# Kernel tuning notes

Measured on AMD Instinct MI355X. Metric: run time of the kernel, lower is better.

The kernel has to match this reference:

```python
import jax, jax.numpy as jnp
import numpy as np

HEADS = 16
D_K = 64  # hidden_units // heads


def setup_inputs() -> dict:
    key = jax.random.key(0)
    ks = jax.random.split(key, 9)
    B, S, D, H = 4, 2048, 1024, 1024  # batch, seq, in_shape, hidden_units
    inputs = jax.random.normal(ks[0], (B, S, D), dtype=jnp.float32)
    # xavier_normal for weights, default bias init ~ small uniform (use zeros for simplicity of baseline? keep uniform like torch)
    def xavier(k, fan_in, fan_out):
        std = jnp.sqrt(2.0 / (fan_in + fan_out))
        return jax.random.normal(k, (fan_out, fan_in), dtype=jnp.float32) * std
    Wq = xavier(ks[1], D, H)
    Wk = xavier(ks[2], D, H)
    Wv = xavier(ks[3], D, H)
    Wo = xavier(ks[4], H, H)
    bound = 1.0 / jnp.sqrt(D)
    bq = jax.random.uniform(ks[5], (H,), minval=-bound, maxval=bound, dtype=jnp.float32)
    bk = jax.random.uniform(ks[6], (H,), minval=-bound, maxval=bound, dtype=jnp.float32)
    bv = jax.random.uniform(ks[7], (H,), minval=-bound, maxval=bound, dtype=jnp.float32)
    bo = jax.random.uniform(ks[8], (H,), minval=-1.0 / jnp.sqrt(H), maxval=1.0 / jnp.sqrt(H), dtype=jnp.float32)
    return {"inputs": inputs, "Wq": Wq, "bq": bq, "Wk": Wk, "bk": bk,
            "Wv": Wv, "bv": bv, "Wo": Wo, "bo": bo}


def reference(inputs, Wq, bq, Wk, bk, Wv, bv, Wo, bo):
    B, S, _ = inputs.shape
    # QKV projections -> (B, S, heads, d_k)
    def proj(W, b):
        return (inputs @ W.T + b).reshape(B, S, HEADS, D_K)
    q = proj(Wq, bq)
    k = proj(Wk, bk)
    v = proj(Wv, bv)
    scale = 1.0 / jnp.sqrt(jnp.float32(D_K))
    # scores: (B, heads, S, S)
    scores = jnp.einsum('bqhd,bkhd->bhqk', q, k) * scale
    attn = jax.nn.softmax(scores, axis=-1)
    # (B, heads, S, d_k) -> (B, S, heads*d_k)
    ctx = jnp.einsum('bhqk,bkhd->bqhd', attn, v).reshape(B, S, HEADS * D_K)
    out = ctx @ Wo.T + bo
    return out
```

## Files before the change

### kernel.cpp

```cpp
#include <hip/hip_runtime.h>
#include <stdint.h>


using bf16x8 = __attribute__((ext_vector_type(8))) short;
using f32x4  = __attribute__((ext_vector_type(4))) float;

#define QSCALE 0.18033688f

__device__ __forceinline__ unsigned short f2bf(float f) {
    unsigned u = __builtin_bit_cast(unsigned, f);
    u += 0x7fffu + ((u >> 16) & 1u);
    return (unsigned short)(u >> 16);
}

__device__ __forceinline__ unsigned pack2bf(float f0, float f1) {
    unsigned u0 = __builtin_bit_cast(unsigned, f0) + 0x8000u;
    unsigned u1 = __builtin_bit_cast(unsigned, f1) + 0x8000u;
    return __builtin_amdgcn_perm(u1, u0, 0x07060302);
}

__device__ __forceinline__ void gld16(const void* g, void* l) {
    void* gnc = (void*)g;
    __builtin_amdgcn_global_load_lds((__attribute__((address_space(1))) void*)gnc,
                                     (__attribute__((address_space(3))) void*)l,
                                     16, 0, 0);
}

__device__ __forceinline__ int swz(int R, int g) {
    return R * 64 + ((g ^ (R & 7)) << 3);
}

__global__ void castall(const float* __restrict__ X, const float* __restrict__ Wq,
                        const float* __restrict__ Wk, const float* __restrict__ Wv,
                        const float* __restrict__ Wo, unsigned short* __restrict__ Xb,
                        unsigned short* __restrict__ Wqkvb, unsigned short* __restrict__ Wob) {
    const int bx = blockIdx.x;
    const float* src; unsigned short* dst; int idx;
    if (bx < 8192) { src = X; dst = Xb; idx = bx * 256 + threadIdx.x; }
    else {
        const int r = bx - 8192, w = r >> 10;
        idx = (r & 1023) * 256 + threadIdx.x;
        src = (w == 0) ? Wq : (w == 1) ? Wk : (w == 2) ? Wv : Wo;
        dst = (w == 3) ? Wob : Wqkvb + (size_t)w * 1048576;
    }
    float4 v = ((const float4*)src)[idx];
    ((uint2*)dst)[idx] = make_uint2(pack2bf(v.x, v.y), pack2bf(v.z, v.w));
}

__global__ __launch_bounds__(256) void gemm_qkv(const unsigned short* __restrict__ A,
                                                const unsigned short* __restrict__ Wqkv,
                                                const float* __restrict__ bq,
                                                const float* __restrict__ bk,
                                                const float* __restrict__ bv,
                                                unsigned short* __restrict__ Qb,
                                                unsigned short* __restrict__ Kb,
                                                unsigned short* __restrict__ Vt) {
    __shared__ alignas(16) unsigned short smem[17408];
    unsigned short* sA = smem;
    unsigned short* sB = smem + 8192;
    unsigned short* OT = smem;

    const int tid  = threadIdx.x;
    const int lane = tid & 63;
    const int wave = tid >> 6;
    const int quad = lane >> 4;
    const int l15  = lane & 15;
    const int lr   = lane >> 3;
    const int lcs  = (((lane & 7) ^ lr) << 3);
    const int nb   = blockIdx.x >> 3;
    const int col0 = (blockIdx.x & 7) * 128;
    const int row0 = blockIdx.y * 128;
    const unsigned short* W = Wqkv + ((size_t)nb << 20);
    const float* bias = (nb == 0) ? bq : (nb == 1) ? bk : bv;
    const int wm = wave >> 1, wn = wave & 1;

    f32x4 acc[4][4];
#pragma unroll
    for (int i = 0; i < 4; i++)
#pragma unroll
        for (int j = 0; j < 4; j++) acc[i][j] = f32x4{0.f, 0.f, 0.f, 0.f};

    for (int kt = 0; kt < 16; ++kt) {
        const int k0 = kt * 64;
#pragma unroll
        for (int i = 0; i < 4; i++) {
            const int c = wave * 4 + i;
            const int r = c * 8 + lr;
            gld16(A + (size_t)(row0 + r) * 1024 + k0 + lcs, &sA[c * 512]);
            gld16(W + (size_t)(col0 + r) * 1024 + k0 + lcs, &sB[c * 512]);
        }
        __syncthreads();
#pragma unroll
        for (int kx = 0; kx < 2; ++kx) {
            bf16x8 a[4], b[4];
#pragma unroll
            for (int i = 0; i < 4; i++) {
                a[i] = *(const bf16x8*)&sA[swz(wm * 64 + i * 16 + l15, kx * 4 + quad)];
                b[i] = *(const bf16x8*)&sB[swz(wn * 64 + i * 16 + l15, kx * 4 + quad)];
            }
#pragma unroll
            for (int i = 0; i < 4; i++)
#pragma unroll
                for (int j = 0; j < 4; j++)
                    acc[i][j] = __builtin_amdgcn_mfma_f32_16x16x32_bf16(a[i], b[j], acc[i][j], 0, 0, 0);
        }
        __syncthreads();
    }

    if (nb != 2) {
        const float sc = (nb == 0) ? QSCALE : 1.0f;
#pragma unroll
        for (int i = 0; i < 4; i++) {
#pragma unroll
            for (int j = 0; j < 4; j++) {
                const int ct  = wn * 64 + j * 16 + l15;
                const float bvv = bias[col0 + ct];
                const int rt  = wm * 64 + i * 16 + quad * 4;
#pragma unroll
                for (int r = 0; r < 4; r++)
                    OT[(rt + r) * 136 + ct] = f2bf((acc[i][j][r] + bvv) * sc);
            }
        }
    } else {
#pragma unroll
        for (int i = 0; i < 4; i++) {
#pragma unroll
            for (int j = 0; j < 4; j++) {
                const int ct  = wn * 64 + j * 16 + l15;
                const float bvv = bias[col0 + ct];
                const int rt  = wm * 64 + i * 16 + quad * 4;
                *(uint2*)&OT[ct * 136 + rt] =
                    make_uint2(pack2bf(acc[i][j][0] + bvv, acc[i][j][1] + bvv),
                               pack2bf(acc[i][j][2] + bvv, acc[i][j][3] + bvv));
            }
        }
    }
    __syncthreads();

    const int rr   = wave * 32 + (lane >> 1);
    const int half = lane & 1;
    if (nb != 2) {
        unsigned short* C = (nb == 0) ? Qb : Kb;
        unsigned short* gdst = C + (size_t)(row0 + rr) * 1024 + col0 + half * 64;
#pragma unroll
        for (int k = 0; k < 8; k++)
            *(bf16x8*)(gdst + k * 8) = *(const bf16x8*)&OT[rr * 136 + half * 64 + k * 8];
    } else {
        const int bb = row0 >> 11, s0l = row0 & 2047;
        unsigned short* gdst = Vt + ((size_t)(bb * 1024 + col0 + rr)) * 2048 + s0l + half * 64;
#pragma unroll
        for (int k = 0; k < 8; k++)
            *(bf16x8*)(gdst + k * 8) = *(const bf16x8*)&OT[rr * 136 + half * 64 + k * 8];
    }
}

__global__ __launch_bounds__(256) void gemm_out(const unsigned short* __restrict__ A,
                                                const unsigned short* __restrict__ W,
                                                const float* __restrict__ bias,
                                                float* __restrict__ C) {
    __shared__ alignas(16) unsigned short sA[128 * 64];
    __shared__ alignas(16) unsigned short sB[128 * 64];
    const int tid  = threadIdx.x;
    const int lane = tid & 63;
    const int wave = tid >> 6;
    const int quad = lane >> 4;
    const int l15  = lane & 15;
    const int lr   = lane >> 3;
    const int lcs  = (((lane & 7) ^ lr) << 3);
    const int row0 = blockIdx.y * 128;
    const int col0 = blockIdx.x * 128;
    const int wm = wave >> 1, wn = wave & 1;

    f32x4 acc[4][4];
#pragma unroll
    for (int i = 0; i < 4; i++)
#pragma unroll
        for (int j = 0; j < 4; j++) acc[i][j] = f32x4{0.f, 0.f, 0.f, 0.f};

    for (int kt = 0; kt < 16; ++kt) {
        const int k0 = kt * 64;
#pragma unroll
        for (int i = 0; i < 4; i++) {
            const int c = wave * 4 + i;
            const int r = c * 8 + lr;
            gld16(A + (size_t)(row0 + r) * 1024 + k0 + lcs, &sA[c * 512]);
            gld16(W + (size_t)(col0 + r) * 1024 + k0 + lcs, &sB[c * 512]);
        }
        __syncthreads();
#pragma unroll
        for (int kx = 0; kx < 2; ++kx) {
            bf16x8 a[4], b[4];
#pragma unroll
            for (int i = 0; i < 4; i++) {
                a[i] = *(const bf16x8*)&sA[swz(wm * 64 + i * 16 + l15, kx * 4 + quad)];
                b[i] = *(const bf16x8*)&sB[swz(wn * 64 + i * 16 + l15, kx * 4 + quad)];
            }
#pragma unroll
            for (int i = 0; i < 4; i++)
#pragma unroll
                for (int j = 0; j < 4; j++)
                    acc[i][j] = __builtin_amdgcn_mfma_f32_16x16x32_bf16(a[i], b[j], acc[i][j], 0, 0, 0);
        }
        __syncthreads();
    }

#pragma unroll
    for (int i = 0; i < 4; i++) {
#pragma unroll
        for (int j = 0; j < 4; j++) {
            const int col   = col0 + wn * 64 + j * 16 + l15;
            const float bvv = bias[col];
            const int rbase = row0 + wm * 64 + i * 16 + quad * 4;
#pragma unroll
            for (int r = 0; r < 4; r++)
                C[(size_t)(rbase + r) * 1024 + col] = acc[i][j][r] + bvv;
        }
    }
}

__global__ __launch_bounds__(256) void attn(const unsigned short* __restrict__ Q,
                                            const unsigned short* __restrict__ K,
                                            const unsigned short* __restrict__ Vt,
                                            unsigned short* __restrict__ Ctx) {
    __shared__ alignas(16) unsigned short Kl[64 * 64];
    __shared__ alignas(16) unsigned short Vl[64 * 64];
    __shared__ alignas(16) unsigned short Pl[4][32][72];

    const int tid  = threadIdx.x;
    const int lane = tid & 63;
    const int wave = tid >> 6;
    const int quad = lane >> 4;
    const int l15  = lane & 15;
    const int lr   = lane >> 3;
    const int lcs  = (((lane & 7) ^ lr) << 3);

    const int qt = blockIdx.x, h = blockIdx.y, b = blockIdx.z;
    const int q0 = qt * 128;
    const size_t tokbase = (size_t)b * 2048;

    bf16x8 qa[2][2];
#pragma unroll
    for (int mt = 0; mt < 2; ++mt)
#pragma unroll
        for (int kx = 0; kx < 2; ++kx)
            qa[mt][kx] = *(const bf16x8*)(Q + (tokbase + q0 + wave * 32 + mt * 16 + l15) * 1024 +
                                          h * 64 + kx * 32 + quad * 8);

    f32x4 O[2][4];
#pragma unroll
    for (int mt = 0; mt < 2; ++mt)
#pragma unroll
        for (int nt = 0; nt < 4; ++nt) O[mt][nt] = f32x4{0.f, 0.f, 0.f, 0.f};
    float rs[2] = {0.f, 0.f};

    for (int kt = 0; kt < 32; ++kt) {
#pragma unroll
        for (int i = 0; i < 2; i++) {
            const int c  = wave * 2 + i;
            const int rr = c * 8 + lr;
            gld16(K + (tokbase + kt * 64 + rr) * 1024 + h * 64 + lcs, &Kl[c * 512]);
            gld16(Vt + ((size_t)(b * 1024 + h * 64 + rr)) * 2048 + kt * 64 + lcs, &Vl[c * 512]);
        }
        __syncthreads();

        f32x4 St[4][2];
#pragma unroll
        for (int nt = 0; nt < 4; ++nt)
#pragma unroll
            for (int mt = 0; mt < 2; ++mt) St[nt][mt] = f32x4{0.f, 0.f, 0.f, 0.f};
#pragma unroll
        for (int kx = 0; kx < 2; ++kx) {
            bf16x8 kb[4];
#pragma unroll
            for (int nt = 0; nt < 4; ++nt)
                kb[nt] = *(const bf16x8*)&Kl[swz(nt * 16 + l15, kx * 4 + quad)];
#pragma unroll
            for (int nt = 0; nt < 4; ++nt)
#pragma unroll
                for (int mt = 0; mt < 2; ++mt)
                    St[nt][mt] = __builtin_amdgcn_mfma_f32_16x16x32_bf16(kb[nt], qa[mt][kx], St[nt][mt], 0, 0, 0);
        }

#pragma unroll
        for (int mt = 0; mt < 2; ++mt) {
            float rsl = 0.f;
#pragma unroll
            for (int nt = 0; nt < 4; ++nt) {
                float p0 = __builtin_amdgcn_exp2f(St[nt][mt][0]);
                float p1 = __builtin_amdgcn_exp2f(St[nt][mt][1]);
                float p2 = __builtin_amdgcn_exp2f(St[nt][mt][2]);
                float p3 = __builtin_amdgcn_exp2f(St[nt][mt][3]);
                rsl += (p0 + p1) + (p2 + p3);
                *(uint2*)&Pl[wave][mt * 16 + l15][nt * 16 + quad * 4] =
                    make_uint2(pack2bf(p0, p1), pack2bf(p2, p3));
            }
            rs[mt] += rsl;
        }

#pragma unroll
        for (int kx = 0; kx < 2; ++kx) {
            bf16x8 pa[2], vb[4];
#pragma unroll
            for (int mt = 0; mt < 2; ++mt)
                pa[mt] = *(const bf16x8*)&Pl[wave][mt * 16 + l15][kx * 32 + quad * 8];
#pragma unroll
            for (int nt = 0; nt < 4; ++nt)
                vb[nt] = *(const bf16x8*)&Vl[swz(nt * 16 + l15, kx * 4 + quad)];
#pragma unroll
            for (int mt = 0; mt < 2; ++mt)
#pragma unroll
                for (int nt = 0; nt < 4; ++nt)
                    O[mt][nt] = __builtin_amdgcn_mfma_f32_16x16x32_bf16(pa[mt], vb[nt], O[mt][nt], 0, 0, 0);
        }
        __syncthreads();
    }

    float linv[2][4];
#pragma unroll
    for (int mt = 0; mt < 2; ++mt) {
        float lv = rs[mt];
        lv += __shfl_xor(lv, 16);
        lv += __shfl_xor(lv, 32);
#pragma unroll
        for (int r = 0; r < 4; ++r)
            linv[mt][r] = 1.0f / __shfl(lv, quad * 4 + r);
    }

#pragma unroll
    for (int mt = 0; mt < 2; ++mt) {
#pragma unroll
        for (int r = 0; r < 4; ++r) {
            const int row   = q0 + wave * 32 + mt * 16 + quad * 4 + r;
            const size_t base = (tokbase + row) * 1024 + h * 64;
#pragma unroll
            for (int nt = 0; nt < 4; ++nt)
                Ctx[base + nt * 16 + l15] = f2bf(O[mt][nt][r] * linv[mt][r]);
        }
    }
}

extern "C" void kernel_launch(void* const* d_in, const int* in_sizes, int n_in,
                              void* d_out, int out_size, void* d_ws, size_t ws_size,
                              hipStream_t stream) {
    (void)in_sizes; (void)n_in; (void)out_size; (void)ws_size;
    const float* X  = (const float*)d_in[0];
    const float* Wq = (const float*)d_in[1];
    const float* bq = (const float*)d_in[2];
    const float* Wk = (const float*)d_in[3];
    const float* bk = (const float*)d_in[4];
    const float* Wv = (const float*)d_in[5];
    const float* bv = (const float*)d_in[6];
    const float* Wo = (const float*)d_in[7];
    const float* bo = (const float*)d_in[8];

    char* ws = (char*)d_ws;
    unsigned short* Xb    = (unsigned short*)(ws);
    unsigned short* Qb    = (unsigned short*)(ws + (size_t)16 * 1048576);
    unsigned short* Kb    = (unsigned short*)(ws + (size_t)32 * 1048576);
    unsigned short* Vt    = (unsigned short*)(ws + (size_t)48 * 1048576);
    unsigned short* Wqkvb = (unsigned short*)(ws + (size_t)64 * 1048576);
    unsigned short* Wob   = (unsigned short*)(ws + (size_t)70 * 1048576);
    unsigned short* Ctx   = Xb;

    castall<<<dim3(12288), 256, 0, stream>>>(X, Wq, Wk, Wv, Wo, Xb, Wqkvb, Wob);
    gemm_qkv<<<dim3(24, 64), 256, 0, stream>>>(Xb, Wqkvb, bq, bk, bv, Qb, Kb, Vt);
    attn<<<dim3(16, 16, 4), 256, 0, stream>>>(Qb, Kb, Vt, Ctx);
    gemm_out<<<dim3(8, 64), 256, 0, stream>>>(Ctx, Wob, bo, (float*)d_out);
}
```

Before: 302.8 us.

## Double-buffer LDS tiles in output GEMM and attention kernels

Both gemm_out and attn now keep two LDS buffers and issue the global-to-LDS loads for the next K tile right after the barrier, before computing on the current tile. The trailing barrier is dropped, so each iteration has one barrier instead of two. The aim is to overlap global memory latency with MFMA work. It doubles LDS use per block, which may reduce occupancy. Correctness depends on the single barrier ordering buffer reuse and on the async LDS loads being complete when the barrier is reached.

```diff
diff --git a/kernel.cpp b/kernel.cpp
--- a/kernel.cpp
+++ b/kernel.cpp
@@ -158,8 +158,8 @@
                                                 const unsigned short* __restrict__ W,
                                                 const float* __restrict__ bias,
                                                 float* __restrict__ C) {
-    __shared__ alignas(16) unsigned short sA[128 * 64];
-    __shared__ alignas(16) unsigned short sB[128 * 64];
+    __shared__ alignas(16) unsigned short sA[2][8192];
+    __shared__ alignas(16) unsigned short sB[2][8192];
     const int tid  = threadIdx.x;
     const int lane = tid & 63;
     const int wave = tid >> 6;
@@ -177,23 +177,30 @@
 #pragma unroll
         for (int j = 0; j < 4; j++) acc[i][j] = f32x4{0.f, 0.f, 0.f, 0.f};
 
+#define GO_STAGE(kt_, buf_)                                                        \
+    {                                                                              \
+        const int k0_ = (kt_) * 64;                                                \
+        _Pragma("unroll")                                                          \
+        for (int i = 0; i < 4; i++) {                                              \
+            const int c = wave * 4 + i;                                            \
+            const int r = c * 8 + lr;                                              \
+            gld16(A + (size_t)(row0 + r) * 1024 + k0_ + lcs, &sA[buf_][c * 512]);  \
+            gld16(W + (size_t)(col0 + r) * 1024 + k0_ + lcs, &sB[buf_][c * 512]);  \
+        }                                                                          \
+    }
+
+    GO_STAGE(0, 0)
     for (int kt = 0; kt < 16; ++kt) {
-        const int k0 = kt * 64;
-#pragma unroll
-        for (int i = 0; i < 4; i++) {
-            const int c = wave * 4 + i;
-            const int r = c * 8 + lr;
-            gld16(A + (size_t)(row0 + r) * 1024 + k0 + lcs, &sA[c * 512]);
-            gld16(W + (size_t)(col0 + r) * 1024 + k0 + lcs, &sB[c * 512]);
-        }
+        const int buf = kt & 1;
         __syncthreads();
+        if (kt < 15) GO_STAGE(kt + 1, buf ^ 1)
 #pragma unroll
         for (int kx = 0; kx < 2; ++kx) {
             bf16x8 a[4], b[4];
 #pragma unroll
             for (int i = 0; i < 4; i++) {
-                a[i] = *(const bf16x8*)&sA[swz(wm * 64 + i * 16 + l15, kx * 4 + quad)];
-                b[i] = *(const bf16x8*)&sB[swz(wn * 64 + i * 16 + l15, kx * 4 + quad)];
+                a[i] = *(const bf16x8*)&sA[buf][swz(wm * 64 + i * 16 + l15, kx * 4 + quad)];
+                b[i] = *(const bf16x8*)&sB[buf][swz(wn * 64 + i * 16 + l15, kx * 4 + quad)];
             }
 #pragma unroll
             for (int i = 0; i < 4; i++)
@@ -201,8 +208,8 @@
                 for (int j = 0; j < 4; j++)
                     acc[i][j] = __builtin_amdgcn_mfma_f32_16x16x32_bf16(a[i], b[j], acc[i][j], 0, 0, 0);
         }
-        __syncthreads();
-    }
+    }
+#undef GO_STAGE
 
 #pragma unroll
     for (int i = 0; i < 4; i++) {
@@ -222,8 +229,8 @@
                                             const unsigned short* __restrict__ K,
                                             const unsigned short* __restrict__ Vt,
                                             unsigned short* __restrict__ Ctx) {
-    __shared__ alignas(16) unsigned short Kl[64 * 64];
-    __shared__ alignas(16) unsigned short Vl[64 * 64];
+    __shared__ alignas(16) unsigned short Kl[2][64 * 64];
+    __shared__ alignas(16) unsigned short Vl[2][64 * 64];
     __shared__ alignas(16) unsigned short Pl[4][32][72];
 
     const int tid  = threadIdx.x;
@@ -253,15 +260,23 @@
         for (int nt = 0; nt < 4; ++nt) O[mt][nt] = f32x4{0.f, 0.f, 0.f, 0.f};
     float rs[2] = {0.f, 0.f};
 
+#define AT_STAGE(kt_, buf_)                                                                     \
+    {                                                                                           \
+        _Pragma("unroll")                                                                       \
+        for (int i = 0; i < 2; i++) {                                                           \
+            const int c  = wave * 2 + i;                                                        \
+            const int rr = c * 8 + lr;                                                          \
+            gld16(K + (tokbase + (kt_) * 64 + rr) * 1024 + h * 64 + lcs, &Kl[buf_][c * 512]);   \
+            gld16(Vt + ((size_t)(b * 1024 + h * 64 + rr)) * 2048 + (kt_) * 64 + lcs,            \
+                  &Vl[buf_][c * 512]);                                                          \
+        }                                                                                       \
+    }
+
+    AT_STAGE(0, 0)
     for (int kt = 0; kt < 32; ++kt) {
-#pragma unroll
-        for (int i = 0; i < 2; i++) {
-            const int c  = wave * 2 + i;
-            const int rr = c * 8 + lr;
-            gld16(K + (tokbase + kt * 64 + rr) * 1024 + h * 64 + lcs, &Kl[c * 512]);
-            gld16(Vt + ((size_t)(b * 1024 + h * 64 + rr)) * 2048 + kt * 64 + lcs, &Vl[c * 512]);
-        }
+        const int buf = kt & 1;
         __syncthreads();
+        if (kt < 31) AT_STAGE(kt + 1, buf ^ 1)
 
         f32x4 St[4][2];
 #pragma unroll
@@ -273,7 +288,7 @@
             bf16x8 kb[4];
 #pragma unroll
             for (int nt = 0; nt < 4; ++nt)
-                kb[nt] = *(const bf16x8*)&Kl[swz(nt * 16 + l15, kx * 4 + quad)];
+                kb[nt] = *(const bf16x8*)&Kl[buf][swz(nt * 16 + l15, kx * 4 + quad)];
 #pragma unroll
             for (int nt = 0; nt < 4; ++nt)
 #pragma unroll
@@ -305,15 +320,15 @@
                 pa[mt] = *(const bf16x8*)&Pl[wave][mt * 16 + l15][kx * 32 + quad * 8];
 #pragma unroll
             for (int nt = 0; nt < 4; ++nt)
-                vb[nt] = *(const bf16x8*)&Vl[swz(nt * 16 + l15, kx * 4 + quad)];
+                vb[nt] = *(const bf16x8*)&Vl[buf][swz(nt * 16 + l15, kx * 4 + quad)];
 #pragma unroll
             for (int mt = 0; mt < 2; ++mt)
 #pragma unroll
                 for (int nt = 0; nt < 4; ++nt)
                     O[mt][nt] = __builtin_amdgcn_mfma_f32_16x16x32_bf16(pa[mt], vb[nt], O[mt][nt], 0, 0, 0);
         }
-        __syncthreads();
-    }
+    }
+#undef AT_STAGE
 
     float linv[2][4];
 #pragma unroll
```

New measurement: 311.8 us. 3.0% more time.

## Double-buffer K/V tiles in attention, widen blocks to 512 threads, MFMA row sums

Applied to the files above, without the earlier changes.

The attention kernel now uses 8 waves per block covering 256 query rows, so each K/V tile loaded into LDS is shared by twice as many waves. K/V tiles are double-buffered, with the next tile prefetched while the current one is computed, which leaves one barrier per iteration instead of two. The softmax denominator is now taken from an extra MFMA against a ones vector, replacing scalar adds and cross-lane shuffles. This costs extra LDS and one extra MFMA per output row tile, and halves the grid to 512 blocks.

```diff
diff --git a/kernel.cpp b/kernel.cpp
--- a/kernel.cpp
+++ b/kernel.cpp
@@ -218,13 +218,13 @@
     }
 }
 
-__global__ __launch_bounds__(256) void attn(const unsigned short* __restrict__ Q,
+__global__ __launch_bounds__(512) void attn(const unsigned short* __restrict__ Q,
                                             const unsigned short* __restrict__ K,
                                             const unsigned short* __restrict__ Vt,
                                             unsigned short* __restrict__ Ctx) {
-    __shared__ alignas(16) unsigned short Kl[64 * 64];
-    __shared__ alignas(16) unsigned short Vl[64 * 64];
-    __shared__ alignas(16) unsigned short Pl[4][32][72];
+    __shared__ alignas(16) unsigned short Kl[2][4096];
+    __shared__ alignas(16) unsigned short Vl[2][4096];
+    __shared__ alignas(16) unsigned short Pl[8][32][72];
 
     const int tid  = threadIdx.x;
     const int lane = tid & 63;
@@ -235,7 +235,7 @@
     const int lcs  = (((lane & 7) ^ lr) << 3);
 
     const int qt = blockIdx.x, h = blockIdx.y, b = blockIdx.z;
-    const int q0 = qt * 128;
+    const int q0 = qt * 256;
     const size_t tokbase = (size_t)b * 2048;
 
     bf16x8 qa[2][2];
@@ -246,22 +246,28 @@
             qa[mt][kx] = *(const bf16x8*)(Q + (tokbase + q0 + wave * 32 + mt * 16 + l15) * 1024 +
                                           h * 64 + kx * 32 + quad * 8);
 
-    f32x4 O[2][4];
-#pragma unroll
-    for (int mt = 0; mt < 2; ++mt)
+    f32x4 O[2][4], Osum[2];
+#pragma unroll
+    for (int mt = 0; mt < 2; ++mt) {
 #pragma unroll
         for (int nt = 0; nt < 4; ++nt) O[mt][nt] = f32x4{0.f, 0.f, 0.f, 0.f};
-    float rs[2] = {0.f, 0.f};
-
+        Osum[mt] = f32x4{0.f, 0.f, 0.f, 0.f};
+    }
+    const bf16x8 vones = {16256, 16256, 16256, 16256, 16256, 16256, 16256, 16256};
+
+#define AT_STAGE(kt_, buf_)                                                                     \
+    {                                                                                           \
+        const int rr = wave * 8 + lr;                                                           \
+        gld16(K + (tokbase + (kt_) * 64 + rr) * 1024 + h * 64 + lcs, &Kl[buf_][wave * 512]);    \
+        gld16(Vt + ((size_t)(b * 1024 + h * 64 + rr)) * 2048 + (kt_) * 64 + lcs,                \
+              &Vl[buf_][wave * 512]);                                                           \
+    }
+
+    AT_STAGE(0, 0)
     for (int kt = 0; kt < 32; ++kt) {
-#pragma unroll
-        for (int i = 0; i < 2; i++) {
-            const int c  = wave * 2 + i;
-            const int rr = c * 8 + lr;
-            gld16(K + (tokbase + kt * 64 + rr) * 1024 + h * 64 + lcs, &Kl[c * 512]);
-            gld16(Vt + ((size_t)(b * 1024 + h * 64 + rr)) * 2048 + kt * 64 + lcs, &Vl[c * 512]);
-        }
-        __syncthreads();
+        const int buf = kt & 1;
+        __syncthreads();
+        if (kt < 31) AT_STAGE(kt + 1, buf ^ 1)
 
         f32x4 St[4][2];
 #pragma unroll
@@ -273,7 +279,7 @@
             bf16x8 kb[4];
 #pragma unroll
             for (int nt = 0; nt < 4; ++nt)
-                kb[nt] = *(const bf16x8*)&Kl[swz(nt * 16 + l15, kx * 4 + quad)];
+                kb[nt] = *(const bf16x8*)&Kl[buf][swz(nt * 16 + l15, kx * 4 + quad)];
 #pragma unroll
             for (int nt = 0; nt < 4; ++nt)
 #pragma unroll
@@ -283,18 +289,15 @@
 
 #pragma unroll
         for (int mt = 0; mt < 2; ++mt) {
-            float rsl = 0.f;
 #pragma unroll
             for (int nt = 0; nt < 4; ++nt) {
                 float p0 = __builtin_amdgcn_exp2f(St[nt][mt][0]);
                 float p1 = __builtin_amdgcn_exp2f(St[nt][mt][1]);
                 float p2 = __builtin_amdgcn_exp2f(St[nt][mt][2]);
                 float p3 = __builtin_amdgcn_exp2f(St[nt][mt][3]);
-                rsl += (p0 + p1) + (p2 + p3);
                 *(uint2*)&Pl[wave][mt * 16 + l15][nt * 16 + quad * 4] =
                     make_uint2(pack2bf(p0, p1), pack2bf(p2, p3));
             }
-            rs[mt] += rsl;
         }
 
 #pragma unroll
@@ -305,36 +308,28 @@
                 pa[mt] = *(const bf16x8*)&Pl[wave][mt * 16 + l15][kx * 32 + quad * 8];
 #pragma unroll
             for (int nt = 0; nt < 4; ++nt)
-                vb[nt] = *(const bf16x8*)&Vl[swz(nt * 16 + l15, kx * 4 + quad)];
-#pragma unroll
-            for (int mt = 0; mt < 2; ++mt)
+                vb[nt] = *(const bf16x8*)&Vl[buf][swz(nt * 16 + l15, kx * 4 + quad)];
+#pragma unroll
+            for (int mt = 0; mt < 2; ++mt) {
 #pragma unroll
                 for (int nt = 0; nt < 4; ++nt)
                     O[mt][nt] = __builtin_amdgcn_mfma_f32_16x16x32_bf16(pa[mt], vb[nt], O[mt][nt], 0, 0, 0);
-        }
-        __syncthreads();
-    }
-
-    float linv[2][4];
+                Osum[mt] = __builtin_amdgcn_mfma_f32_16x16x32_bf16(pa[mt], vones, Osum[mt], 0, 0, 0);
+            }
+        }
+    }
+#undef AT_STAGE
+
 #pragma unroll
     for (int mt = 0; mt < 2; ++mt) {
-        float lv = rs[mt];
-        lv += __shfl_xor(lv, 16);
-        lv += __shfl_xor(lv, 32);
-#pragma unroll
-        for (int r = 0; r < 4; ++r)
-            linv[mt][r] = 1.0f / __shfl(lv, quad * 4 + r);
-    }
-
-#pragma unroll
-    for (int mt = 0; mt < 2; ++mt) {
 #pragma unroll
         for (int r = 0; r < 4; ++r) {
+            const float inv = 1.0f / Osum[mt][r];
             const int row   = q0 + wave * 32 + mt * 16 + quad * 4 + r;
             const size_t base = (tokbase + row) * 1024 + h * 64;
 #pragma unroll
             for (int nt = 0; nt < 4; ++nt)
-                Ctx[base + nt * 16 + l15] = f2bf(O[mt][nt][r] * linv[mt][r]);
+                Ctx[base + nt * 16 + l15] = f2bf(O[mt][nt][r] * inv);
         }
     }
 }
@@ -364,6 +359,6 @@
 
     castall<<<dim3(12288), 256, 0, stream>>>(X, Wq, Wk, Wv, Wo, Xb, Wqkvb, Wob);
     gemm_qkv<<<dim3(24, 64), 256, 0, stream>>>(Xb, Wqkvb, bq, bk, bv, Qb, Kb, Vt);
-    attn<<<dim3(16, 16, 4), 256, 0, stream>>>(Qb, Kb, Vt, Ctx);
+    attn<<<dim3(8, 16, 4), 512, 0, stream>>>(Qb, Kb, Vt, Ctx);
     gemm_out<<<dim3(8, 64), 256, 0, stream>>>(Ctx, Wob, bo, (float*)d_out);
 }
```

Result: faster. 281.4 us (-7.0%).
